# Kernel tuning notes

Measured on AMD Instinct MI355X. Metric: run time of the kernel, lower is better.

The kernel has to match this reference:

```python
import jax, jax.numpy as jnp
import numpy as np

B, T, D, H = 2, 2048, 1024, 16
DH = D // H
PD = 6
_PAIRS = [(0, 1), (0, 2), (0, 3), (1, 2), (1, 3), (2, 3)]
_J6 = jnp.array([[0, 0, 0, 0, 0, 1], [0, 0, 0, 0, -1, 0], [0, 0, 0, 1, 0, 0],
                 [0, 0, 1, 0, 0, 0], [0, -1, 0, 0, 0, 0], [1, 0, 0, 0, 0, 0]], dtype=jnp.float32)


def exterior(p1, p2):
    # Plucker line coordinates of the 2-plane spanned by p1,p2 in R^4, normalized.
    parts = [p1[..., i] * p2[..., j] - p1[..., j] * p2[..., i] for i, j in _PAIRS]
    L = jnp.stack(parts, axis=-1)
    n = jnp.linalg.norm(L, axis=-1, keepdims=True)
    return L / jnp.maximum(n, 1e-12)


def setup_inputs() -> dict:
    key = jax.random.key(0)
    ks = jax.random.split(key, 12)
    s = 0.02
    A = 0.99 * jnp.broadcast_to(jnp.eye(PD, dtype=jnp.float32), (H, PD, PD))
    return {
        'x': jax.random.normal(ks[0], (B, T, D), jnp.float32),
        'Wqkv': jax.random.normal(ks[1], (D, 3 * D), jnp.float32) * s,
        'bqkv': jnp.zeros((3 * D,), jnp.float32),
        'W1w': jax.random.normal(ks[2], (D, 4 * H), jnp.float32) * s,
        'W2w': jax.random.normal(ks[3], (D, 4 * H), jnp.float32) * s,
        'W1r': jax.random.normal(ks[4], (D, 4 * H), jnp.float32) * s,
        'W2r': jax.random.normal(ks[5], (D, 4 * H), jnp.float32) * s,
        'Wmv': jax.random.normal(ks[6], (D, D), jnp.float32) * s,
        'bmv': jnp.zeros((D,), jnp.float32),
        'Wg': jax.random.normal(ks[7], (D, H), jnp.float32) * s,
        'bg': jnp.zeros((H,), jnp.float32),
        'mem_scale': jnp.full((H,), 0.1, jnp.float32),
        'Wout': jax.random.normal(ks[8], (D, D), jnp.float32) * s,
        'bout': jnp.zeros((D,), jnp.float32),
        'A': A,
    }


def reference(x, Wqkv, bqkv, W1w, W2w, W1r, W2r, Wmv, bmv, Wg, bg, mem_scale, Wout, bout, A):
    Bx, Tx, Dx = x.shape
    # ---- causal softmax attention ----
    qkv = (x @ Wqkv + bqkv).reshape(Bx, Tx, 3, H, DH).transpose(2, 0, 3, 1, 4)
    q, k, v = qkv[0], qkv[1], qkv[2]            # (B,H,T,dh)
    scores = jnp.einsum('bhtd,bhsd->bhts', q, k) * (DH ** -0.5)
    mask = jnp.triu(jnp.ones((Tx, Tx), bool), 1)
    scores = jnp.where(mask, -jnp.inf, scores)
    attn = jax.nn.softmax(scores, axis=-1)      # dropout is identity in eval
    seq_out = jnp.einsum('bhts,bhsd->bthd', attn, v).reshape(Bx, Tx, Dx)
    # ---- write/read lines (Plucker) ----
    x_prev = jnp.concatenate([jnp.zeros((Bx, 1, Dx), x.dtype), x[:, :-1]], axis=1)
    w1 = (x_prev @ W1w).reshape(Bx, Tx, H, 4)
    w2 = (x @ W2w).reshape(Bx, Tx, H, 4)
    write_lines = exterior(w1, w2)              # (B,T,H,6)
    r1 = (x @ W1r).reshape(Bx, Tx, H, 4)
    r2 = (x @ W2r).reshape(Bx, Tx, H, 4)
    read_lines = exterior(r1, r2)               # (B,T,H,6)
    Jw = jnp.einsum('bthi,ij->bthj', write_lines, _J6)
    Jw_T = Jw.transpose(1, 0, 2, 3)             # (T,B,H,6)
    rd_T = read_lines.transpose(1, 0, 2, 3)     # (T,B,H,6)
    # ---- Riccati-style state scan: M_t = A M_{t-1} A^T + Jw_t Jw_t^T ----
    def step(M, ts):
        rd_t, Jw_t = ts                          # (B,H,6)
        score = jnp.einsum('bhp,bhpq,bhq->bh', rd_t, M, rd_t)
        M = jnp.einsum('hpq,bhqr,hsr->bhps', A, M, A) + Jw_t[..., :, None] * Jw_t[..., None, :]
        return M, score
    M0 = jnp.zeros((Bx, H, PD, PD), x.dtype)
    _, scores_T = jax.lax.scan(step, M0, (rd_T, Jw_T))   # (T,B,H)
    mem_score_t = scores_T.transpose(1, 0, 2)            # (B,T,H)
    # ---- gated memory readout ----
    mem_val = x @ Wmv + bmv
    gate = jax.nn.sigmoid(x @ Wg + bg)                   # (B,T,H)
    gated = jax.nn.sigmoid(mem_score_t * mem_scale[None, None, :]) * gate
    gated = gated.mean(axis=-1, keepdims=True)           # (B,T,1)
    return (seq_out + gated * mem_val) @ Wout + bout
```

## Files before the change

kernel.cpp:

```cpp
#include <hip/hip_runtime.h>
#include <cstdint>
#include <cstddef>

typedef unsigned short u16;
typedef unsigned int u32;
typedef __attribute__((ext_vector_type(4))) float f32x4;
typedef __attribute__((ext_vector_type(4))) float float4v;
typedef __attribute__((ext_vector_type(8))) short short8;

#define LDC 4368

__device__ __forceinline__ float bf2f(u16 u){ return __uint_as_float(((u32)u) << 16); }
__device__ __forceinline__ u16 f2bf(float f){
  u32 x = __float_as_uint(f);
  x += 0x7FFFu + ((x >> 16) & 1u);
  return (u16)(x >> 16);
}
__device__ __forceinline__ u16 f2bf_rhu(float f){
  return (u16)((__float_as_uint(f) + 0x8000u) >> 16);
}
#if __has_builtin(__builtin_amdgcn_exp2f)
#define EXP2(x) __builtin_amdgcn_exp2f(x)
#else
#define EXP2(x) exp2f(x)
#endif
__device__ __forceinline__ void mfma16(f32x4& d, short8 a, short8 b){
  d = __builtin_amdgcn_mfma_f32_16x16x32_bf16(a, b, d, 0, 0, 0);
}
__device__ __forceinline__ void async_lds16(void* lds, const void* g){
  __builtin_amdgcn_global_load_lds((const __attribute__((address_space(1))) u32*)g,
                                   (__attribute__((address_space(3))) u32*)lds, 16, 0, 0);
}
__device__ __forceinline__ float sigm(float x){ return 1.f / (1.f + __expf(-x)); }
__device__ __forceinline__ void storev(u16* p, float v){ *p = f2bf(v); }
__device__ __forceinline__ void storev(float* p, float v){ *p = v; }

__device__ __forceinline__ void t32(const float* __restrict__ src, u16* __restrict__ dst,
                                    int R, int Ccols, int c0, int r0, int tid, u16 tile[32][33])
{
  int tx = tid & 31, ty0 = tid >> 5;
  #pragma unroll
  for (int i = 0; i < 4; i++){
    int r = r0 + ty0 + i * 8, c = c0 + tx;
    u16 v = 0;
    if (r < R && c < Ccols) v = f2bf(src[(size_t)r * Ccols + c]);
    tile[ty0 + i * 8][tx] = v;
  }
  __syncthreads();
  #pragma unroll
  for (int i = 0; i < 4; i++){
    int cc = c0 + ty0 + i * 8, rr = r0 + tx;
    if (cc < Ccols && rr < R) dst[(size_t)cc * R + rr] = tile[tx][ty0 + i * 8];
  }
}

__global__ __launch_bounds__(256) void prep_kernel(
    const float* __restrict__ x, const float* __restrict__ bqkv, const float* __restrict__ bmv,
    const float* __restrict__ bg, const float* __restrict__ Wqkv,
    const float* __restrict__ W1w, const float* __restrict__ W2w,
    const float* __restrict__ W1r, const float* __restrict__ W2r,
    const float* __restrict__ Wmv, const float* __restrict__ Wout, const float* __restrict__ Wg,
    u16* __restrict__ xb, float* __restrict__ biasfull, u16* __restrict__ BT, u16* __restrict__ WoutT)
{
  __shared__ u16 tile[32][33];
  const int b = blockIdx.x, tid = threadIdx.x;
  if (b < 2048){
    int i = b * 256 + tid;
    float4v a = *(const float4v*)(x + (size_t)i * 8);
    float4v c = *(const float4v*)(x + (size_t)i * 8 + 4);
    short8 o;
    #pragma unroll
    for (int j = 0; j < 4; j++){ o[j] = (short)f2bf(a[j]); o[4 + j] = (short)f2bf(c[j]); }
    *(short8*)(xb + (size_t)i * 8) = o;
  } else if (b < 2066){
    int i = (b - 2048) * 256 + tid;
    if (i < 4368){
      float v;
      if (i < 3072) v = bqkv[i];
      else if (i < 3328) v = 0.f;
      else if (i < 4352) v = bmv[i - 3328];
      else v = bg[i - 4352];
      biasfull[i] = v;
    }
  } else if (b < 5138){
    int local = b - 2066;
    t32(Wqkv, BT, 1024, 3072, (local % 96) * 32, (local / 96) * 32, tid, tile);
  } else if (b < 5394){
    int local = b - 5138;
    int z = local >> 6, rem = local & 63;
    const float* src = (z == 0) ? W1w : (z == 1) ? W2w : (z == 2) ? W1r : W2r;
    t32(src, BT + (size_t)(3072 + z * 64) * 1024, 1024, 64, (rem & 1) * 32, (rem >> 1) * 32, tid, tile);
  } else if (b < 7442){
    int local = b - 5394;
    int z = local >> 10, rem = local & 1023;
    const float* src = z ? Wout : Wmv;
    u16* dst = z ? WoutT : (BT + (size_t)3328 * 1024);
    t32(src, dst, 1024, 1024, (rem & 31) * 32, (rem >> 5) * 32, tid, tile);
  } else {
    int local = b - 7442;
    t32(Wg, BT + (size_t)4352 * 1024, 1024, 16, 0, local * 32, tid, tile);
  }
}

template<typename OT>
__global__ __launch_bounds__(256) void gemm_bt(const u16* __restrict__ Ag, const u16* __restrict__ BTg,
                                               const float* __restrict__ bias, OT* __restrict__ Cg,
                                               int M, int N, int K, int ldc)
{
  __shared__ __align__(16) u16 As[2][128 * 32];
  __shared__ __align__(16) u16 Bs[2][128 * 32];
  const int tid = threadIdx.x, lane = tid & 63, w = tid >> 6;
  const int l15 = lane & 15, l4 = lane >> 4;
  const int qx = gridDim.x >> 3, bid = blockIdx.x;
  const int fid = (bid & 7) * qx + (bid >> 3);
  const int m0 = (fid & 31) * 128, n0 = (fid >> 5) * 128;
  const int wr = w >> 1, wc = w & 1;
  f32x4 acc[4][4] = {};
  const u16* aP[2]; const u16* bP[2];
  #pragma unroll
  for (int j = 0; j < 2; j++){
    int i = w * 128 + j * 64 + lane;
    int lrow = i >> 3, cc = i & 7;
    int sc = cc ^ (lrow & 7);
    int grow = lrow * 2 + (sc >> 2);
    int ka = (sc & 3) * 8;
    aP[j] = Ag + (size_t)(m0 + grow) * K + ka;
    int rb = n0 + grow; if (rb > N - 1) rb = N - 1;
    bP[j] = BTg + (size_t)rb * K + ka;
  }
  const int nk = K >> 5;
  #pragma unroll
  for (int j = 0; j < 2; j++){
    async_lds16((char*)As[0] + w * 2048 + j * 1024, aP[j]);
    async_lds16((char*)Bs[0] + w * 2048 + j * 1024, bP[j]);
  }
  __syncthreads();
  for (int t = 0; t < nk; t++){
    const int cur = t & 1;
    if (t + 1 < nk){
      const int k0 = (t + 1) << 5;
      char* An = (char*)As[cur ^ 1] + w * 2048;
      char* Bn = (char*)Bs[cur ^ 1] + w * 2048;
      #pragma unroll
      for (int j = 0; j < 2; j++){
        async_lds16(An + j * 1024, aP[j] + k0);
        async_lds16(Bn + j * 1024, bP[j] + k0);
      }
    }
    const char* Ab = (const char*)As[cur];
    const char* Bb = (const char*)Bs[cur];
    short8 a[4], b[4];
    #pragma unroll
    for (int mi = 0; mi < 4; mi++){
      int r = wr * 64 + mi * 16 + l15;
      int lrow = r >> 1;
      int slot = (((r & 1) << 2) + l4) ^ (lrow & 7);
      a[mi] = *(const short8*)(Ab + lrow * 128 + slot * 16);
    }
    #pragma unroll
    for (int ni = 0; ni < 4; ni++){
      int r = wc * 64 + ni * 16 + l15;
      int lrow = r >> 1;
      int slot = (((r & 1) << 2) + l4) ^ (lrow & 7);
      b[ni] = *(const short8*)(Bb + lrow * 128 + slot * 16);
    }
    #pragma unroll
    for (int mi = 0; mi < 4; mi++)
      #pragma unroll
      for (int ni = 0; ni < 4; ni++)
        mfma16(acc[mi][ni], a[mi], b[ni]);
    __syncthreads();
  }
  #pragma unroll
  for (int mi = 0; mi < 4; mi++){
    #pragma unroll
    for (int ni = 0; ni < 4; ni++){
      int col = n0 + wc * 64 + ni * 16 + l15;
      if (col < N){
        float bv = bias ? bias[col] : 0.f;
        #pragma unroll
        for (int r = 0; r < 4; r++){
          int row = m0 + wr * 64 + mi * 16 + l4 * 4 + r;
          storev(&Cg[(size_t)row * ldc + col], acc[mi][ni][r] + bv);
        }
      }
    }
  }
}

__device__ __forceinline__ void ext6(float* L, const float* p, const float* q){
  L[0] = p[0]*q[1] - p[1]*q[0];
  L[1] = p[0]*q[2] - p[2]*q[0];
  L[2] = p[0]*q[3] - p[3]*q[0];
  L[3] = p[1]*q[2] - p[2]*q[1];
  L[4] = p[1]*q[3] - p[3]*q[1];
  L[5] = p[2]*q[3] - p[3]*q[2];
  float n = sqrtf(L[0]*L[0]+L[1]*L[1]+L[2]*L[2]+L[3]*L[3]+L[4]*L[4]+L[5]*L[5]);
  float inv = 1.f / fmaxf(n, 1e-12f);
  #pragma unroll
  for (int i = 0; i < 6; i++) L[i] *= inv;
}

__global__ __launch_bounds__(256) void lines_powers_kernel(const u16* __restrict__ C, const float* __restrict__ Ain,
                                                           float* __restrict__ rd, float* __restrict__ Jw,
                                                           float* __restrict__ Gk)
{
  __shared__ float Af[36], Cur[36];
  const int blk = blockIdx.x, tid = threadIdx.x;
  if (blk < 256){
    int idx = blk * 256 + tid;
    int h = idx & 15, t = (idx >> 4) & 2047, b = idx >> 15;
    size_t m = (size_t)b * 2048 + t;
    float w1[4] = {0.f, 0.f, 0.f, 0.f}, w2[4], r1[4], r2[4];
    if (t > 0){
      const u16* p = C + (m - 1) * LDC + 3072 + h * 4;
      #pragma unroll
      for (int i = 0; i < 4; i++) w1[i] = bf2f(p[i]);
    }
    {
      const u16* p = C + m * LDC + 3136 + h * 4;
      #pragma unroll
      for (int i = 0; i < 4; i++) w2[i] = bf2f(p[i]);
      p = C + m * LDC + 3200 + h * 4;
      #pragma unroll
      for (int i = 0; i < 4; i++) r1[i] = bf2f(p[i]);
      p = C + m * LDC + 3264 + h * 4;
      #pragma unroll
      for (int i = 0; i < 4; i++) r2[i] = bf2f(p[i]);
    }
    float L[6], R[6];
    ext6(L, w1, w2);
    ext6(R, r1, r2);
    size_t o = ((size_t)(b * 16 + h) * 2048 + t) * 6;
    #pragma unroll
    for (int i = 0; i < 6; i++) rd[o + i] = R[i];
    Jw[o + 0] =  L[5];
    Jw[o + 1] = -L[4];
    Jw[o + 2] =  L[3];
    Jw[o + 3] =  L[2];
    Jw[o + 4] = -L[1];
    Jw[o + 5] =  L[0];
  } else {
    const int h = blk - 256;
    const int p = tid / 6, q = tid % 6;
    if (tid < 36){
      Af[tid] = Ain[h * 36 + tid];
      float id = (p == q) ? 1.f : 0.f;
      Cur[tid] = id;
      Gk[(size_t)h * 65 * 36 + tid] = id;
    }
    __syncthreads();
    for (int k = 1; k <= 64; k++){
      float v = 0.f;
      if (tid < 36){
        #pragma unroll
        for (int j = 0; j < 6; j++) v += Cur[p * 6 + j] * Af[j * 6 + q];
      }
      __syncthreads();
      if (tid < 36){
        Cur[tid] = v;
        Gk[((size_t)h * 65 + k) * 36 + tid] = v;
      }
      __syncthreads();
    }
  }
}

__global__ __launch_bounds__(256) void chunk_tv_kernel(const float* __restrict__ Jw, const float* __restrict__ Ain,
                                                       float* __restrict__ Sb, const u16* __restrict__ C,
                                                       u16* __restrict__ VT)
{
  __shared__ float Jl[4][384];
  __shared__ float Af[4][36], Ml[4][36], Nl[4][36];
  __shared__ u16 tile[32][33];
  const int blk = blockIdx.x, tid = threadIdx.x;
  if (blk < 256){
    const int g = tid >> 6, lt = tid & 63;
    const int task = blk * 4 + g;
    const int c = task & 31, bh = task >> 5, h = bh & 15;
    const int p = lt / 6, q = lt % 6;
    for (int i = lt; i < 384; i += 64) Jl[g][i] = Jw[((size_t)bh * 2048 + c * 64) * 6 + i];
    if (lt < 36){ Af[g][lt] = Ain[h * 36 + lt]; Ml[g][lt] = 0.f; }
    __syncthreads();
    float arow[6], acol[6];
    if (lt < 36){
      #pragma unroll
      for (int k = 0; k < 6; k++){ arow[k] = Af[g][p * 6 + k]; acol[k] = Af[g][q * 6 + k]; }
    }
    for (int s = 0; s < 64; s++){
      float n = 0.f;
      if (lt < 36){
        #pragma unroll
        for (int k = 0; k < 6; k++) n += arow[k] * Ml[g][k * 6 + q];
        Nl[g][lt] = n;
      }
      __syncthreads();
      if (lt < 36){
        float m = Jl[g][s * 6 + p] * Jl[g][s * 6 + q];
        #pragma unroll
        for (int k = 0; k < 6; k++) m += Nl[g][p * 6 + k] * acol[k];
        Ml[g][lt] = m;
      }
      __syncthreads();
    }
    if (lt < 36) Sb[((size_t)bh * 32 + c) * 36 + lt] = Ml[g][lt];
  } else {
    int local = blk - 256;
    int bh = local >> 7, rem = local & 127;
    int b = bh >> 4, h = bh & 15;
    const u16* src = C + (size_t)b * 2048 * LDC + 2048 + h * 64;
    int c0 = (rem & 1) * 32, r0 = (rem >> 1) * 32;
    int tx = tid & 31, ty0 = tid >> 5;
    #pragma unroll
    for (int i = 0; i < 4; i++)
      tile[ty0 + i * 8][tx] = src[(size_t)(r0 + ty0 + i * 8) * LDC + c0 + tx];
    __syncthreads();
    u16* dstb = VT + (size_t)bh * 64 * 2048;
    #pragma unroll
    for (int i = 0; i < 4; i++)
      dstb[(size_t)(c0 + ty0 + i * 8) * 2048 + r0 + tx] = tile[tx][ty0 + i * 8];
  }
}

__global__ __launch_bounds__(64) void boundary_kernel(const float* __restrict__ Sb, const float* __restrict__ Gk,
                                                      float* __restrict__ Bb)
{
  __shared__ float A64[36], Bl[36], Nl[36];
  const int bh = blockIdx.x, h = bh & 15;
  const int tid = threadIdx.x;
  const int p = tid / 6, q = tid % 6;
  if (tid < 36){ A64[tid] = Gk[((size_t)h * 65 + 64) * 36 + tid]; Bl[tid] = 0.f; }
  __syncthreads();
  float arow[6], acol[6];
  if (tid < 36){
    #pragma unroll
    for (int k = 0; k < 6; k++){ arow[k] = A64[p * 6 + k]; acol[k] = A64[q * 6 + k]; }
  }
  for (int c = 0; c < 32; c++){
    if (tid < 36) Bb[((size_t)bh * 32 + c) * 36 + tid] = Bl[tid];
    float n = 0.f;
    if (tid < 36){
      #pragma unroll
      for (int k = 0; k < 6; k++) n += arow[k] * Bl[k * 6 + q];
    }
    __syncthreads();
    if (tid < 36) Nl[tid] = n;
    __syncthreads();
    if (tid < 36){
      float m = Sb[((size_t)bh * 32 + c) * 36 + tid];
      #pragma unroll
      for (int k = 0; k < 6; k++) m += Nl[p * 6 + k] * acol[k];
      Bl[tid] = m;
    }
    __syncthreads();
  }
}

__global__ __launch_bounds__(256) void attn_score_kernel(const u16* __restrict__ C, const u16* __restrict__ VT,
                                                         u16* __restrict__ seqb,
                                                         const float* __restrict__ rd, const float* __restrict__ Jw,
                                                         const float* __restrict__ Gk, const float* __restrict__ Bb,
                                                         float* __restrict__ score)
{
  __shared__ __align__(16) char smem[24576];
  const int blk = blockIdx.x, tid = threadIdx.x;
  if (blk < 1024){
    u16* Ks = (u16*)smem;
    u16* Vs = (u16*)(smem + 8192);
    const int bh = blk & 31, bb = bh >> 4, h = bh & 15;
    const int qblk = 31 - (blk >> 5);
    const int lane = tid & 63, w = tid >> 6;
    const int l15 = lane & 15, l4 = lane >> 4;
    u16* Psw = (u16*)(smem + 16384) + w * 1024;
    const int q0 = qblk * 64 + w * 16;
    const float csc = 0.1803368801f;
    const u16* qb = C + (size_t)(bb * 2048 + q0 + l15) * LDC + h * 64 + l4 * 8;
    short8 qf0 = *(const short8*)qb;
    short8 qf1 = *(const short8*)(qb + 32);
    #pragma unroll
    for (int j = 0; j < 8; j++){
      qf0[j] = (short)f2bf(bf2f((u16)qf0[j]) * csc);
      qf1[j] = (short)f2bf(bf2f((u16)qf1[j]) * csc);
    }
    f32x4 o[4] = {};
    float mrun[4], lsum[4];
    #pragma unroll
    for (int r = 0; r < 4; r++){ mrun[r] = -1e30f; lsum[r] = 0.f; }
    const int nkv = qblk + 1;
    const int rowA = tid >> 3, chA = tid & 7;
    const int swA = chA ^ (rowA & 7);
    const u16* Kg = C + (size_t)(bb * 2048) * LDC + 1024 + h * 64 + chA * 8;
    const u16* Vg = VT + ((size_t)bh * 64 + rowA) * 2048 + chA * 8;
    short8 kr0, kr1, vr0, vr1;
    {
      kr0 = *(const short8*)(Kg + (size_t)rowA * LDC);
      kr1 = *(const short8*)(Kg + (size_t)(rowA + 32) * LDC);
      vr0 = *(const short8*)(Vg);
      vr1 = *(const short8*)(Vg + 32 * 2048);
    }
    for (int i = 0; i < nkv; i++){
      const int kv0 = i * 64;
      __syncthreads();
      *(short8*)((char*)Ks + rowA * 128 + swA * 16)        = kr0;
      *(short8*)((char*)Ks + (rowA + 32) * 128 + swA * 16) = kr1;
      *(short8*)((char*)Vs + rowA * 128 + swA * 16)        = vr0;
      *(short8*)((char*)Vs + (rowA + 32) * 128 + swA * 16) = vr1;
      __syncthreads();
      if (i + 1 < nkv){
        int nx = kv0 + 64;
        kr0 = *(const short8*)(Kg + (size_t)(nx + rowA) * LDC);
        kr1 = *(const short8*)(Kg + (size_t)(nx + rowA + 32) * LDC);
        vr0 = *(const short8*)(Vg + nx);
        vr1 = *(const short8*)(Vg + nx + 32 * 2048);
      }
      const bool diag = (i == qblk);
      f32x4 s4[4] = {};
      #pragma unroll
      for (int j = 0; j < 4; j++){
        const int srow = j * 16 + l15, rm = srow & 7;
        const char* base = (const char*)Ks + srow * 128;
        short8 b0 = *(const short8*)(base + ((l4 ^ rm) << 4));
        short8 b1 = *(const short8*)(base + (((4 + l4) ^ rm) << 4));
        mfma16(s4[j], qf0, b0);
        mfma16(s4[j], qf1, b1);
      }
      float ps[4][4], lm[4];
      #pragma unroll
      for (int r = 0; r < 4; r++){
        float v0 = s4[0][r], v1 = s4[1][r], v2 = s4[2][r], v3 = s4[3][r];
        if (diag){
          int qrow = w * 16 + l4 * 4 + r;
          if (l15 > qrow)      v0 = -1e30f;
          if (16 + l15 > qrow) v1 = -1e30f;
          if (32 + l15 > qrow) v2 = -1e30f;
          if (48 + l15 > qrow) v3 = -1e30f;
        }
        lm[r] = fmaxf(fmaxf(v0, v1), fmaxf(v2, v3));
        ps[r][0] = v0; ps[r][1] = v1; ps[r][2] = v2; ps[r][3] = v3;
      }
      int ok = (lm[0] <= mrun[0] + 11.5f) && (lm[1] <= mrun[1] + 11.5f)
            && (lm[2] <= mrun[2] + 11.5f) && (lm[3] <= mrun[3] + 11.5f);
      if (!__all(ok)){
        #pragma unroll
        for (int r = 0; r < 4; r++){
          float mx = lm[r];
          mx = fmaxf(mx, __shfl_xor(mx, 1));
          mx = fmaxf(mx, __shfl_xor(mx, 2));
          mx = fmaxf(mx, __shfl_xor(mx, 4));
          mx = fmaxf(mx, __shfl_xor(mx, 8));
          float mnew = fmaxf(mrun[r], mx);
          float sc = EXP2(mrun[r] - mnew);
          mrun[r] = mnew;
          lsum[r] *= sc;
          o[0][r] *= sc; o[1][r] *= sc; o[2][r] *= sc; o[3][r] *= sc;
        }
      }
      #pragma unroll
      for (int r = 0; r < 4; r++){
        float p0 = EXP2(ps[r][0] - mrun[r]);
        float p1 = EXP2(ps[r][1] - mrun[r]);
        float p2 = EXP2(ps[r][2] - mrun[r]);
        float p3 = EXP2(ps[r][3] - mrun[r]);
        lsum[r] += (p0 + p1) + (p2 + p3);
        ps[r][0] = p0; ps[r][1] = p1; ps[r][2] = p2; ps[r][3] = p3;
      }
      char* pw = (char*)Psw;
      const int cb = (l15 & 7) * 2;
      #pragma unroll
      for (int r = 0; r < 4; r++){
        const int prow = l4 * 4 + r, rm = prow & 7;
        char* prb = pw + prow * 128 + cb;
        #pragma unroll
        for (int j = 0; j < 4; j++){
          int cj = (j * 2 + (l15 >> 3)) ^ rm;
          *((u16*)(prb + cj * 16)) = f2bf_rhu(ps[r][j]);
        }
      }
      const int prm = l15 & 7;
      short8 pa0 = *(const short8*)(pw + l15 * 128 + ((l4 ^ prm) << 4));
      short8 pa1 = *(const short8*)(pw + l15 * 128 + (((4 + l4) ^ prm) << 4));
      #pragma unroll
      for (int j = 0; j < 4; j++){
        const int drow = j * 16 + l15, rm = drow & 7;
        const char* vb = (const char*)Vs + drow * 128;
        short8 b0 = *(const short8*)(vb + ((l4 ^ rm) << 4));
        short8 b1 = *(const short8*)(vb + (((4 + l4) ^ rm) << 4));
        mfma16(o[j], pa0, b0);
        mfma16(o[j], pa1, b1);
      }
    }
    #pragma unroll
    for (int r = 0; r < 4; r++){
      float ls = lsum[r];
      ls += __shfl_xor(ls, 1);
      ls += __shfl_xor(ls, 2);
      ls += __shfl_xor(ls, 4);
      ls += __shfl_xor(ls, 8);
      float inv = 1.f / ls;
      size_t base = (size_t)(bb * 2048 + q0 + l4 * 4 + r) * 1024 + h * 64;
      seqb[base + l15]      = f2bf(o[0][r] * inv);
      seqb[base + 16 + l15] = f2bf(o[1][r] * inv);
      seqb[base + 32 + l15] = f2bf(o[2][r] * inv);
      seqb[base + 48 + l15] = f2bf(o[3][r] * inv);
    }
  } else {
    float* Gl = (float*)smem;
    float* Jl = (float*)(smem + 9216);
    float* Bl = (float*)(smem + 16896);
    const int local = blk - 1024;
    const int tblk = local & 7, bh = local >> 3, h = bh & 15;
    const int t0 = tblk * 256;
    for (int i = tid; i < 64 * 36; i += 256) Gl[i] = Gk[(size_t)h * 65 * 36 + i];
    {
      int base = t0 * 6 - 384;
      for (int i = tid; i < 1920; i += 256){
        int s6 = base + i;
        Jl[i] = (s6 >= 0) ? Jw[(size_t)bh * (2048 * 6) + s6] : 0.f;
      }
    }
    for (int i = tid; i < 144; i += 256) Bl[i] = Bb[((size_t)bh * 32 + tblk * 4) * 36 + i];
    __syncthreads();
    float Ar[36];
    #pragma unroll
    for (int i = 0; i < 36; i++) Ar[i] = Gl[36 + i];
    const int t = t0 + tid;
    const int cl = tid >> 6;
    const int dlt = tid & 63;
    float rdv[6];
    {
      const float* rp = rd + ((size_t)bh * 2048 + t) * 6;
      #pragma unroll
      for (int q = 0; q < 6; q++) rdv[q] = rp[q];
    }
    const float* g = Gl + dlt * 36;
    float u[6];
    #pragma unroll
    for (int p = 0; p < 6; p++){
      float s = 0.f;
      #pragma unroll
      for (int q = 0; q < 6; q++) s += rdv[q] * g[q * 6 + p];
      u[p] = s;
    }
    float acc = 0.f;
    #pragma unroll
    for (int p = 0; p < 6; p++){
      float bv = 0.f;
      #pragma unroll
      for (int q = 0; q < 6; q++) bv += Bl[cl * 36 + p * 6 + q] * u[q];
      acc += u[p] * bv;
    }
    float wv[6];
    #pragma unroll
    for (int q = 0; q < 6; q++) wv[q] = rdv[q];
    const int sIdx = tid + 63;
    for (int k = 0; k < dlt; k++){
      const float* jp = Jl + (sIdx - k) * 6;
      float uu = wv[0]*jp[0] + wv[1]*jp[1] + wv[2]*jp[2] + wv[3]*jp[3] + wv[4]*jp[4] + wv[5]*jp[5];
      acc += uu * uu;
      float nw[6];
      #pragma unroll
      for (int q = 0; q < 6; q++)
        nw[q] = wv[0]*Ar[q] + wv[1]*Ar[6+q] + wv[2]*Ar[12+q] + wv[3]*Ar[18+q] + wv[4]*Ar[24+q] + wv[5]*Ar[30+q];
      #pragma unroll
      for (int q = 0; q < 6; q++) wv[q] = nw[q];
    }
    score[(size_t)bh * 2048 + t] = acc;
  }
}

__global__ __launch_bounds__(256) void gated_combine_kernel(const float* __restrict__ score, const u16* __restrict__ C,
                                                            const float* __restrict__ mem_scale,
                                                            const u16* __restrict__ seqb, u16* __restrict__ preb)
{
  __shared__ float gsh[2];
  const int blk = blockIdx.x, tid = threadIdx.x;
  const int m0 = blk * 2;
  if (tid < 2){
    int m = m0 + tid;
    int b = m >> 11, t = m & 2047;
    float acc = 0.f;
    for (int h2 = 0; h2 < 16; h2++){
      float sc = score[(size_t)(b * 16 + h2) * 2048 + t];
      float ms = mem_scale[h2];
      float gp = bf2f(C[(size_t)m * LDC + 4352 + h2]);
      acc += sigm(sc * ms) * sigm(gp);
    }
    gsh[tid] = acc * (1.f / 16.f);
  }
  __syncthreads();
  const int m = m0 + (tid >> 7), d8 = (tid & 127) * 8;
  const float g = gsh[tid >> 7];
  short8 sv = *(const short8*)(seqb + (size_t)m * 1024 + d8);
  short8 mv = *(const short8*)(C + (size_t)m * LDC + 3328 + d8);
  short8 ov;
  #pragma unroll
  for (int j = 0; j < 8; j++){
    float f = bf2f((u16)sv[j]) + g * bf2f((u16)mv[j]);
    ov[j] = (short)f2bf(f);
  }
  *(short8*)(preb + (size_t)m * 1024 + d8) = ov;
}

extern "C" void kernel_launch(void* const* d_in, const int* in_sizes, int n_in,
                              void* d_out, int out_size, void* d_ws, size_t ws_size,
                              hipStream_t stream)
{
  (void)in_sizes; (void)n_in; (void)out_size; (void)ws_size;
  const float* x     = (const float*)d_in[0];
  const float* Wqkv  = (const float*)d_in[1];
  const float* bqkv  = (const float*)d_in[2];
  const float* W1w   = (const float*)d_in[3];
  const float* W2w   = (const float*)d_in[4];
  const float* W1r   = (const float*)d_in[5];
  const float* W2r   = (const float*)d_in[6];
  const float* Wmv   = (const float*)d_in[7];
  const float* bmv   = (const float*)d_in[8];
  const float* Wg    = (const float*)d_in[9];
  const float* bg    = (const float*)d_in[10];
  const float* mem_scale = (const float*)d_in[11];
  const float* Wout  = (const float*)d_in[12];
  const float* bout  = (const float*)d_in[13];
  const float* Am    = (const float*)d_in[14];
  float* out = (float*)d_out;

  char* p = (char*)d_ws;
  auto carve = [&](size_t bytes) -> void* {
    void* r = (void*)p;
    p += (bytes + 255) & ~(size_t)255;
    return r;
  };
  u16*   xb       = (u16*)  carve((size_t)4096 * 1024 * 2);
  u16*   C        = (u16*)  carve((size_t)4096 * LDC * 2);
  u16*   BT       = (u16*)  carve((size_t)LDC * 1024 * 2);
  u16*   WoutT    = (u16*)  carve((size_t)1024 * 1024 * 2);
  float* biasfull = (float*)carve((size_t)LDC * 4);
  u16*   VTb      = (u16*)  carve((size_t)32 * 64 * 2048 * 2);
  u16*   seqb     = (u16*)  carve((size_t)4096 * 1024 * 2);
  float* rdb      = (float*)carve((size_t)32 * 2048 * 6 * 4);
  float* Jwb      = (float*)carve((size_t)32 * 2048 * 6 * 4);
  float* Gk       = (float*)carve((size_t)16 * 65 * 36 * 4);
  float* Sbb      = (float*)carve((size_t)32 * 32 * 36 * 4);
  float* Bbb      = (float*)carve((size_t)32 * 32 * 36 * 4);
  float* scoreb   = (float*)carve((size_t)32 * 2048 * 4);
  u16*   preb     = (u16*)  carve((size_t)4096 * 1024 * 2);

  prep_kernel<<<7474, 256, 0, stream>>>(x, bqkv, bmv, bg, Wqkv, W1w, W2w, W1r, W2r,
                                        Wmv, Wout, Wg, xb, biasfull, BT, WoutT);

  gemm_bt<u16><<<1120, 256, 0, stream>>>(xb, BT, biasfull, C, 4096, LDC, 1024, LDC);

  lines_powers_kernel<<<272, 256, 0, stream>>>(C, Am, rdb, Jwb, Gk);
  chunk_tv_kernel<<<4352, 256, 0, stream>>>(Jwb, Am, Sbb, C, VTb);
  boundary_kernel<<<32, 64, 0, stream>>>(Sbb, Gk, Bbb);
  attn_score_kernel<<<1280, 256, 0, stream>>>(C, VTb, seqb, rdb, Jwb, Gk, Bbb, scoreb);
  gated_combine_kernel<<<2048, 256, 0, stream>>>(scoreb, C, mem_scale, seqb, preb);

  gemm_bt<float><<<256, 256, 0, stream>>>(preb, WoutT, bout, out, 4096, 1024, 1024, 1024);
}
```

Before: 201.9 us.

## Double-buffer K/V tiles in attention and stage bf16 GEMM epilogue through LDS

The attention loop now keeps two LDS buffers for K and V and writes the next tile while the current one is consumed. This removes one of the two barriers per iteration and hides global-load latency better. Separately, the bf16 GEMM epilogue stages the output tile in swizzled shared memory and writes full 16-byte rows, so global stores are coalesced. The cost is more LDS per attention block (40 KB), which may lower occupancy, plus an extra barrier and LDS round trip in the GEMM epilogue.

```diff
diff --git a/kernel.cpp b/kernel.cpp
--- a/kernel.cpp
+++ b/kernel.cpp
@@ -107,8 +107,7 @@
                                                const float* __restrict__ bias, OT* __restrict__ Cg,
                                                int M, int N, int K, int ldc)
 {
-  __shared__ __align__(16) u16 As[2][128 * 32];
-  __shared__ __align__(16) u16 Bs[2][128 * 32];
+  __shared__ __align__(16) char SMEM[32768];
   const int tid = threadIdx.x, lane = tid & 63, w = tid >> 6;
   const int l15 = lane & 15, l4 = lane >> 4;
   const int qx = gridDim.x >> 3, bid = blockIdx.x;
@@ -131,24 +130,24 @@
   const int nk = K >> 5;
   #pragma unroll
   for (int j = 0; j < 2; j++){
-    async_lds16((char*)As[0] + w * 2048 + j * 1024, aP[j]);
-    async_lds16((char*)Bs[0] + w * 2048 + j * 1024, bP[j]);
+    async_lds16(SMEM + w * 2048 + j * 1024, aP[j]);
+    async_lds16(SMEM + 16384 + w * 2048 + j * 1024, bP[j]);
   }
   __syncthreads();
   for (int t = 0; t < nk; t++){
     const int cur = t & 1;
     if (t + 1 < nk){
       const int k0 = (t + 1) << 5;
-      char* An = (char*)As[cur ^ 1] + w * 2048;
-      char* Bn = (char*)Bs[cur ^ 1] + w * 2048;
+      char* An = SMEM + (cur ^ 1) * 8192 + w * 2048;
+      char* Bn = SMEM + 16384 + (cur ^ 1) * 8192 + w * 2048;
       #pragma unroll
       for (int j = 0; j < 2; j++){
         async_lds16(An + j * 1024, aP[j] + k0);
         async_lds16(Bn + j * 1024, bP[j] + k0);
       }
     }
-    const char* Ab = (const char*)As[cur];
-    const char* Bb = (const char*)Bs[cur];
+    const char* Ab = SMEM + cur * 8192;
+    const char* Bb = SMEM + 16384 + cur * 8192;
     short8 a[4], b[4];
     #pragma unroll
     for (int mi = 0; mi < 4; mi++){
@@ -171,17 +170,47 @@
         mfma16(acc[mi][ni], a[mi], b[ni]);
     __syncthreads();
   }
-  #pragma unroll
-  for (int mi = 0; mi < 4; mi++){
-    #pragma unroll
-    for (int ni = 0; ni < 4; ni++){
-      int col = n0 + wc * 64 + ni * 16 + l15;
-      if (col < N){
-        float bv = bias ? bias[col] : 0.f;
+  if constexpr (sizeof(OT) == 2){
+    #pragma unroll
+    for (int mi = 0; mi < 4; mi++){
+      #pragma unroll
+      for (int ni = 0; ni < 4; ni++){
+        int col = wc * 64 + ni * 16 + l15;
+        float bv = bias ? bias[n0 + col] : 0.f;
+        int chunk = col >> 3, ce = col & 7;
         #pragma unroll
         for (int r = 0; r < 4; r++){
-          int row = m0 + wr * 64 + mi * 16 + l4 * 4 + r;
-          storev(&Cg[(size_t)row * ldc + col], acc[mi][ni][r] + bv);
+          int row = wr * 64 + mi * 16 + l4 * 4 + r;
+          *(u16*)(SMEM + row * 256 + ((chunk ^ (row & 15)) << 4) + (ce << 1)) = f2bf(acc[mi][ni][r] + bv);
+        }
+      }
+    }
+    __syncthreads();
+    const int rrow = tid >> 1, half = tid & 1;
+    OT* dst = Cg + (size_t)(m0 + rrow) * ldc + n0 + half * 64;
+    #pragma unroll
+    for (int i = 0; i < 8; i++){
+      int colb = n0 + half * 64 + i * 8;
+      short8 v = *(const short8*)(SMEM + rrow * 256 + (((half * 8 + i) ^ (rrow & 15)) << 4));
+      if (colb + 8 <= N) *(short8*)(dst + i * 8) = v;
+      else {
+        #pragma unroll
+        for (int e = 0; e < 8; e++) if (colb + e < N) dst[i * 8 + e] = (u16)(unsigned short)v[e];
+      }
+    }
+  } else {
+    #pragma unroll
+    for (int mi = 0; mi < 4; mi++){
+      #pragma unroll
+      for (int ni = 0; ni < 4; ni++){
+        int col = n0 + wc * 64 + ni * 16 + l15;
+        if (col < N){
+          float bv = bias ? bias[col] : 0.f;
+          #pragma unroll
+          for (int r = 0; r < 4; r++){
+            int row = m0 + wr * 64 + mi * 16 + l4 * 4 + r;
+            storev(&Cg[(size_t)row * ldc + col], acc[mi][ni][r] + bv);
+          }
         }
       }
     }
@@ -362,16 +391,16 @@
                                                          const float* __restrict__ Gk, const float* __restrict__ Bb,
                                                          float* __restrict__ score)
 {
-  __shared__ __align__(16) char smem[24576];
+  __shared__ __align__(16) char smem[40960];
   const int blk = blockIdx.x, tid = threadIdx.x;
   if (blk < 1024){
-    u16* Ks = (u16*)smem;
-    u16* Vs = (u16*)(smem + 8192);
+    char* KsB = smem;
+    char* VsB = smem + 16384;
     const int bh = blk & 31, bb = bh >> 4, h = bh & 15;
     const int qblk = 31 - (blk >> 5);
     const int lane = tid & 63, w = tid >> 6;
     const int l15 = lane & 15, l4 = lane >> 4;
-    u16* Psw = (u16*)(smem + 16384) + w * 1024;
+    u16* Psw = (u16*)(smem + 32768) + w * 1024;
     const int q0 = qblk * 64 + w * 16;
     const float csc = 0.1803368801f;
     const u16* qb = C + (size_t)(bb * 2048 + q0 + l15) * LDC + h * 64 + l4 * 8;
@@ -392,33 +421,46 @@
     const u16* Kg = C + (size_t)(bb * 2048) * LDC + 1024 + h * 64 + chA * 8;
     const u16* Vg = VT + ((size_t)bh * 64 + rowA) * 2048 + chA * 8;
     short8 kr0, kr1, vr0, vr1;
-    {
-      kr0 = *(const short8*)(Kg + (size_t)rowA * LDC);
-      kr1 = *(const short8*)(Kg + (size_t)(rowA + 32) * LDC);
-      vr0 = *(const short8*)(Vg);
-      vr1 = *(const short8*)(Vg + 32 * 2048);
+    kr0 = *(const short8*)(Kg + (size_t)rowA * LDC);
+    kr1 = *(const short8*)(Kg + (size_t)(rowA + 32) * LDC);
+    vr0 = *(const short8*)(Vg);
+    vr1 = *(const short8*)(Vg + 32 * 2048);
+    *(short8*)(KsB + rowA * 128 + swA * 16)        = kr0;
+    *(short8*)(KsB + (rowA + 32) * 128 + swA * 16) = kr1;
+    *(short8*)(VsB + rowA * 128 + swA * 16)        = vr0;
+    *(short8*)(VsB + (rowA + 32) * 128 + swA * 16) = vr1;
+    if (nkv > 1){
+      kr0 = *(const short8*)(Kg + (size_t)(64 + rowA) * LDC);
+      kr1 = *(const short8*)(Kg + (size_t)(64 + rowA + 32) * LDC);
+      vr0 = *(const short8*)(Vg + 64);
+      vr1 = *(const short8*)(Vg + 64 + 32 * 2048);
     }
     for (int i = 0; i < nkv; i++){
-      const int kv0 = i * 64;
-      __syncthreads();
-      *(short8*)((char*)Ks + rowA * 128 + swA * 16)        = kr0;
-      *(short8*)((char*)Ks + (rowA + 32) * 128 + swA * 16) = kr1;
-      *(short8*)((char*)Vs + rowA * 128 + swA * 16)        = vr0;
-      *(short8*)((char*)Vs + (rowA + 32) * 128 + swA * 16) = vr1;
+      const int cur = i & 1;
       __syncthreads();
       if (i + 1 < nkv){
-        int nx = kv0 + 64;
-        kr0 = *(const short8*)(Kg + (size_t)(nx + rowA) * LDC);
-        kr1 = *(const short8*)(Kg + (size_t)(nx + rowA + 32) * LDC);
-        vr0 = *(const short8*)(Vg + nx);
-        vr1 = *(const short8*)(Vg + nx + 32 * 2048);
-      }
+        char* Kd = KsB + (cur ^ 1) * 8192;
+        char* Vd = VsB + (cur ^ 1) * 8192;
+        *(short8*)(Kd + rowA * 128 + swA * 16)        = kr0;
+        *(short8*)(Kd + (rowA + 32) * 128 + swA * 16) = kr1;
+        *(short8*)(Vd + rowA * 128 + swA * 16)        = vr0;
+        *(short8*)(Vd + (rowA + 32) * 128 + swA * 16) = vr1;
+        if (i + 2 < nkv){
+          int nx = (i + 2) * 64;
+          kr0 = *(const short8*)(Kg + (size_t)(nx + rowA) * LDC);
+          kr1 = *(const short8*)(Kg + (size_t)(nx + rowA + 32) * LDC);
+          vr0 = *(const short8*)(Vg + nx);
+          vr1 = *(const short8*)(Vg + nx + 32 * 2048);
+        }
+      }
+      const char* Ks = KsB + cur * 8192;
+      const char* Vs = VsB + cur * 8192;
       const bool diag = (i == qblk);
       f32x4 s4[4] = {};
       #pragma unroll
       for (int j = 0; j < 4; j++){
         const int srow = j * 16 + l15, rm = srow & 7;
-        const char* base = (const char*)Ks + srow * 128;
+        const char* base = Ks + srow * 128;
         short8 b0 = *(const short8*)(base + ((l4 ^ rm) << 4));
         short8 b1 = *(const short8*)(base + (((4 + l4) ^ rm) << 4));
         mfma16(s4[j], qf0, b0);
@@ -482,7 +524,7 @@
       #pragma unroll
       for (int j = 0; j < 4; j++){
         const int drow = j * 16 + l15, rm = drow & 7;
-        const char* vb = (const char*)Vs + drow * 128;
+        const char* vb = Vs + drow * 128;
         short8 b0 = *(const short8*)(vb + ((l4 ^ rm) << 4));
         short8 b1 = *(const short8*)(vb + (((4 + l4) ^ rm) << 4));
         mfma16(o[j], pa0, b0);
```

Result: slower. 207.1 us (+2.6%).

## Double-buffer K/V shared tiles in attention loop and raise MFMA wave priority

Applied to the files above, without the earlier changes.

Shared memory for K and V becomes double-buffered, so each iteration writes the next tile into the alternate buffer and issues global loads two tiles ahead. This cuts one of the two block-wide barriers per KV iteration and gives global loads more time to land. The MFMA sections are also wrapped in s_setprio to favour matrix work across waves. Shared memory per block grows from 24 KB to 40 KB, which may lower occupancy.

```diff
diff --git a/kernel.cpp b/kernel.cpp
--- a/kernel.cpp
+++ b/kernel.cpp
@@ -362,16 +362,16 @@
                                                          const float* __restrict__ Gk, const float* __restrict__ Bb,
                                                          float* __restrict__ score)
 {
-  __shared__ __align__(16) char smem[24576];
+  __shared__ __align__(16) char smem[40960];
   const int blk = blockIdx.x, tid = threadIdx.x;
   if (blk < 1024){
-    u16* Ks = (u16*)smem;
-    u16* Vs = (u16*)(smem + 8192);
+    char* KsB = smem;
+    char* VsB = smem + 16384;
     const int bh = blk & 31, bb = bh >> 4, h = bh & 15;
     const int qblk = 31 - (blk >> 5);
     const int lane = tid & 63, w = tid >> 6;
     const int l15 = lane & 15, l4 = lane >> 4;
-    u16* Psw = (u16*)(smem + 16384) + w * 1024;
+    u16* Psw = (u16*)(smem + 32768) + w * 1024;
     const int q0 = qblk * 64 + w * 16;
     const float csc = 0.1803368801f;
     const u16* qb = C + (size_t)(bb * 2048 + q0 + l15) * LDC + h * 64 + l4 * 8;
@@ -392,38 +392,53 @@
     const u16* Kg = C + (size_t)(bb * 2048) * LDC + 1024 + h * 64 + chA * 8;
     const u16* Vg = VT + ((size_t)bh * 64 + rowA) * 2048 + chA * 8;
     short8 kr0, kr1, vr0, vr1;
-    {
-      kr0 = *(const short8*)(Kg + (size_t)rowA * LDC);
-      kr1 = *(const short8*)(Kg + (size_t)(rowA + 32) * LDC);
-      vr0 = *(const short8*)(Vg);
-      vr1 = *(const short8*)(Vg + 32 * 2048);
+    kr0 = *(const short8*)(Kg + (size_t)rowA * LDC);
+    kr1 = *(const short8*)(Kg + (size_t)(rowA + 32) * LDC);
+    vr0 = *(const short8*)(Vg);
+    vr1 = *(const short8*)(Vg + 32 * 2048);
+    *(short8*)(KsB + rowA * 128 + swA * 16)        = kr0;
+    *(short8*)(KsB + (rowA + 32) * 128 + swA * 16) = kr1;
+    *(short8*)(VsB + rowA * 128 + swA * 16)        = vr0;
+    *(short8*)(VsB + (rowA + 32) * 128 + swA * 16) = vr1;
+    if (nkv > 1){
+      kr0 = *(const short8*)(Kg + (size_t)(64 + rowA) * LDC);
+      kr1 = *(const short8*)(Kg + (size_t)(64 + rowA + 32) * LDC);
+      vr0 = *(const short8*)(Vg + 64);
+      vr1 = *(const short8*)(Vg + 64 + 32 * 2048);
     }
     for (int i = 0; i < nkv; i++){
-      const int kv0 = i * 64;
-      __syncthreads();
-      *(short8*)((char*)Ks + rowA * 128 + swA * 16)        = kr0;
-      *(short8*)((char*)Ks + (rowA + 32) * 128 + swA * 16) = kr1;
-      *(short8*)((char*)Vs + rowA * 128 + swA * 16)        = vr0;
-      *(short8*)((char*)Vs + (rowA + 32) * 128 + swA * 16) = vr1;
+      const int cur = i & 1;
       __syncthreads();
       if (i + 1 < nkv){
-        int nx = kv0 + 64;
-        kr0 = *(const short8*)(Kg + (size_t)(nx + rowA) * LDC);
-        kr1 = *(const short8*)(Kg + (size_t)(nx + rowA + 32) * LDC);
-        vr0 = *(const short8*)(Vg + nx);
-        vr1 = *(const short8*)(Vg + nx + 32 * 2048);
-      }
+        char* Kd = KsB + (cur ^ 1) * 8192;
+        char* Vd = VsB + (cur ^ 1) * 8192;
+        *(short8*)(Kd + rowA * 128 + swA * 16)        = kr0;
+        *(short8*)(Kd + (rowA + 32) * 128 + swA * 16) = kr1;
+        *(short8*)(Vd + rowA * 128 + swA * 16)        = vr0;
+        *(short8*)(Vd + (rowA + 32) * 128 + swA * 16) = vr1;
+        if (i + 2 < nkv){
+          int nx = (i + 2) * 64;
+          kr0 = *(const short8*)(Kg + (size_t)(nx + rowA) * LDC);
+          kr1 = *(const short8*)(Kg + (size_t)(nx + rowA + 32) * LDC);
+          vr0 = *(const short8*)(Vg + nx);
+          vr1 = *(const short8*)(Vg + nx + 32 * 2048);
+        }
+      }
+      const char* Ks = KsB + cur * 8192;
+      const char* Vs = VsB + cur * 8192;
       const bool diag = (i == qblk);
       f32x4 s4[4] = {};
+      __builtin_amdgcn_s_setprio(1);
       #pragma unroll
       for (int j = 0; j < 4; j++){
         const int srow = j * 16 + l15, rm = srow & 7;
-        const char* base = (const char*)Ks + srow * 128;
+        const char* base = Ks + srow * 128;
         short8 b0 = *(const short8*)(base + ((l4 ^ rm) << 4));
         short8 b1 = *(const short8*)(base + (((4 + l4) ^ rm) << 4));
         mfma16(s4[j], qf0, b0);
         mfma16(s4[j], qf1, b1);
       }
+      __builtin_amdgcn_s_setprio(0);
       float ps[4][4], lm[4];
       #pragma unroll
       for (int r = 0; r < 4; r++){
@@ -479,15 +494,17 @@
       const int prm = l15 & 7;
       short8 pa0 = *(const short8*)(pw + l15 * 128 + ((l4 ^ prm) << 4));
       short8 pa1 = *(const short8*)(pw + l15 * 128 + (((4 + l4) ^ prm) << 4));
+      __builtin_amdgcn_s_setprio(1);
       #pragma unroll
       for (int j = 0; j < 4; j++){
         const int drow = j * 16 + l15, rm = drow & 7;
-        const char* vb = (const char*)Vs + drow * 128;
+        const char* vb = Vs + drow * 128;
         short8 b0 = *(const short8*)(vb + ((l4 ^ rm) << 4));
         short8 b1 = *(const short8*)(vb + (((4 + l4) ^ rm) << 4));
         mfma16(o[j], pa0, b0);
         mfma16(o[j], pa1, b1);
       }
+      __builtin_amdgcn_s_setprio(0);
     }
     #pragma unroll
     for (int r = 0; r < 4; r++){
```

Result: no change. 198.4 us (-1.7%).
